# Optimization experiments

Hardware: AMD Instinct MI355X
Metric: run time of the kernel (lower is better)

Reference implementation:

```python
import jax, jax.numpy as jnp
import numpy as np

N_NODES = 50000
IN_NF = 64
HID = 128
OUT_NF = 64
EDGE_HID = HID // 2  # edge_nf_ratio = 2
N_LAYERS = 4
N_EDGES = 800000
NUM_LATENT_NODES = 64
C_EVEN = 1.0
C_ODD = 2.0 / NUM_LATENT_NODES


def setup_inputs() -> dict:
    key = jax.random.key(0)
    ks = jax.random.split(key, 24)
    def lin(k, fan_in, fan_out):
        # torch nn.Linear default init: U(-1/sqrt(fan_in), 1/sqrt(fan_in))
        bound = 1.0 / np.sqrt(fan_in)
        kw, kb = jax.random.split(k)
        w = jax.random.uniform(kw, (fan_in, fan_out), jnp.float32, -bound, bound)
        b = jax.random.uniform(kb, (fan_out,), jnp.float32, -bound, bound)
        return w, b

    h = jax.random.normal(ks[0], (N_NODES, IN_NF), jnp.float32)
    edges_a = jax.random.randint(ks[1], (2, N_EDGES), 0, N_NODES, jnp.int32)
    edges_b = jax.random.randint(ks[2], (2, N_EDGES), 0, N_NODES, jnp.int32)
    update_mask_a = jax.random.randint(ks[3], (N_NODES, 1), 0, 2, jnp.int32).astype(bool)
    update_mask_b = jax.random.randint(ks[4], (N_NODES, 1), 0, 2, jnp.int32).astype(bool)

    emb_in_w, emb_in_b = lin(ks[5], IN_NF, HID)
    emb_out_w, emb_out_b = lin(ks[6], HID, OUT_NF)

    ew1, eb1, ew2, eb2 = [], [], [], []
    nw1, nb1, nw2, nb2 = [], [], [], []
    for i in range(N_LAYERS):
        w, b = lin(ks[7 + i], 2 * HID, EDGE_HID); ew1.append(w); eb1.append(b)
        w, b = lin(ks[11 + i], EDGE_HID, EDGE_HID); ew2.append(w); eb2.append(b)
        w, b = lin(ks[15 + i], HID + EDGE_HID, HID); nw1.append(w); nb1.append(b)
        w, b = lin(ks[19 + i], HID, HID); nw2.append(w); nb2.append(b)

    stack = lambda xs: jnp.stack(xs, 0)
    return {
        "h": h, "edges_a": edges_a, "edges_b": edges_b,
        "update_mask_a": update_mask_a, "update_mask_b": update_mask_b,
        "emb_in_w": emb_in_w, "emb_in_b": emb_in_b,
        "emb_out_w": emb_out_w, "emb_out_b": emb_out_b,
        "edge_w1": stack(ew1), "edge_b1": stack(eb1),
        "edge_w2": stack(ew2), "edge_b2": stack(eb2),
        "node_w1": stack(nw1), "node_b1": stack(nb1),
        "node_w2": stack(nw2), "node_b2": stack(nb2),
    }


def _gcl(h, edges, mask, C, ew1, eb1, ew2, eb2, nw1, nb1, nw2, nb2):
    row, col = edges[0], edges[1]
    # edge model: gather source/target node feats -> 2-layer SiLU MLP
    feat = jnp.concatenate([h[row], h[col]], axis=-1)      # [E, 2*HID]
    m = jax.nn.silu(feat @ ew1 + eb1)                      # [E, EDGE_HID]
    m = jax.nn.silu(m @ ew2 + eb2)                         # [E, EDGE_HID]
    # aggregate messages to receiving nodes (scatter-add), scaled by C
    agg = jax.ops.segment_sum(m, row, num_segments=h.shape[0]) * C
    # node model with residual
    upd = jax.nn.silu(jnp.concatenate([h, agg], axis=-1) @ nw1 + nb1) @ nw2 + nb2
    h_new = h + upd
    # masked asynchronous update: only nodes with mask=True are updated
    return jnp.where(mask, h_new, h)


def reference(h, edges_a, edges_b, update_mask_a, update_mask_b,
              emb_in_w, emb_in_b, emb_out_w, emb_out_b,
              edge_w1, edge_b1, edge_w2, edge_b2,
              node_w1, node_b1, node_w2, node_b2):
    h = h @ emb_in_w + emb_in_b
    for i in range(N_LAYERS):
        if i % 2 == 0:
            edges, mask, C = edges_a, update_mask_a, C_EVEN
        else:
            edges, mask, C = edges_b, update_mask_b, C_ODD
        h = _gcl(h, edges, mask, C,
                 edge_w1[i], edge_b1[i], edge_w2[i], edge_b2[i],
                 node_w1[i], node_b1[i], node_w2[i], node_b2[i])
    h = h @ emb_out_w + emb_out_b
    return h
```

## Files before the change

### kernel.cpp

```cpp
#include <hip/hip_runtime.h>
#include <cstdint>

typedef __bf16 bf16_t;
typedef bf16_t bf16x8 __attribute__((ext_vector_type(8)));
typedef float floatx4 __attribute__((ext_vector_type(4)));
typedef unsigned short ushort4v __attribute__((ext_vector_type(4)));

constexpr int N_NODES = 50000;
constexpr int N_EDGES = 800000;
constexpr int HID = 128;
constexpr int EH = 64;
constexpr int NCH = (N_NODES + 255) / 256;

__device__ __forceinline__ float silu_f(float x) {
    return x * __builtin_amdgcn_rcpf(1.0f + __expf(-x));
}

__global__ __launch_bounds__(256) void pack_all_kernel(
    const float* __restrict__ embin, const float* __restrict__ embout,
    const float* __restrict__ ew1, const float* __restrict__ ew2,
    const float* __restrict__ nw1, const float* __restrict__ nw2,
    bf16_t* __restrict__ pk)
{
    int t = blockIdx.x * 256 + threadIdx.x;
    const float* W; int K, Nc; int base; bf16_t* out;
    if (t < 1024)       { W = embin;  K = 64;  Nc = 128; base = 0;     out = pk; }
    else if (t < 2048)  { W = embout; K = 128; Nc = 64;  base = 1024;  out = pk + 8192; }
    else if (t < 10240) { W = ew1;    K = 256; Nc = 64;  base = 2048;  out = pk + 16384; }
    else if (t < 12288) { W = ew2;    K = 64;  Nc = 64;  base = 10240; out = pk + 81920; }
    else if (t < 24576) { W = nw1;    K = 192; Nc = 128; base = 12288; out = pk + 98304; }
    else                { W = nw2;    K = 128; Nc = 128; base = 24576; out = pk + 196608; }
    t -= base;
    int KS = K >> 5, NT = Nc >> 4;
    int lane = t & 63;
    int chunk = t >> 6;
    int ks = chunk % KS;
    int nt = (chunk / KS) % NT;
    int l  = chunk / (KS * NT);
    int quad = lane >> 4, coln = lane & 15;
    const float* Wl = W + l * K * Nc;
    bf16x8 v;
#pragma unroll
    for (int j = 0; j < 8; j++)
        v[j] = (bf16_t)Wl[(ks * 32 + quad * 8 + j) * Nc + nt * 16 + coln];
    *(bf16x8*)(out + t * 8) = v;
}

__global__ void hist2_kernel(const int* __restrict__ ea, const int* __restrict__ eb,
                             const int* __restrict__ ma, const int* __restrict__ mb,
                             int* __restrict__ ba, int* __restrict__ bb) {
    int half = gridDim.x >> 1;
    int b = blockIdx.x;
    const int* erows; const int* mask; int* bins;
    if (b < half) { erows = ea; mask = ma; bins = ba; }
    else          { erows = eb; mask = mb; bins = bb; b -= half; }
    int i = b * 256 + threadIdx.x;
    if (i >= N_EDGES) return;
    int r = erows[i];
    if (mask[r] != 0) atomicAdd(&bins[r], 1);
}

__global__ __launch_bounds__(256) void scan_phase1(
    const int* __restrict__ bins_a, const int* __restrict__ bins_b,
    int* __restrict__ bs_a, int* __restrict__ bs_b) {
    const int* bins = blockIdx.y ? bins_b : bins_a;
    int* bs = blockIdx.y ? bs_b : bs_a;
    int i = blockIdx.x * 256 + threadIdx.x;
    int v = (i < N_NODES) ? (bins[i] != 0 ? bins[i] : 0) : 0;
#pragma unroll
    for (int off = 32; off; off >>= 1) v += __shfl_down(v, off, 64);
    __shared__ int ws_[4];
    int lane = threadIdx.x & 63, wv = threadIdx.x >> 6;
    if (lane == 0) ws_[wv] = v;
    __syncthreads();
    if (threadIdx.x == 0) bs[blockIdx.x] = ws_[0] + ws_[1] + ws_[2] + ws_[3];
}

__global__ __launch_bounds__(256) void scan_phase2(
    int* __restrict__ bs_a, int* __restrict__ bs_b,
    int* __restrict__ bins_a, int* __restrict__ bins_b) {
    int* bs = blockIdx.x ? bs_b : bs_a;
    int* bins = blockIdx.x ? bins_b : bins_a;
    int t = threadIdx.x, lane = t & 63, wv = t >> 6;
    int v = (t < NCH) ? bs[t] : 0;
    int s = v;
#pragma unroll
    for (int off = 1; off < 64; off <<= 1) {
        int u = __shfl_up(s, off, 64);
        if (lane >= off) s += u;
    }
    __shared__ int wsum[4];
    if (lane == 63) wsum[wv] = s;
    __syncthreads();
    int woff = 0;
    for (int w = 0; w < wv; w++) woff += wsum[w];
    int excl = s - v + woff;
    if (t < NCH) bs[t] = excl;
    if (t == NCH - 1) bins[N_NODES] = excl + v;
}

__global__ __launch_bounds__(256) void mask_scan2(
    int* __restrict__ ms_a, int* __restrict__ ms_b,
    int* __restrict__ cnt_a, int* __restrict__ cnt_b) {
    int* ms = blockIdx.x ? ms_b : ms_a;
    int* cnt = blockIdx.x ? cnt_b : cnt_a;
    int t = threadIdx.x, lane = t & 63, wv = t >> 6;
    int v = (t < NCH) ? ms[t] : 0;
    int s = v;
#pragma unroll
    for (int off = 1; off < 64; off <<= 1) {
        int u = __shfl_up(s, off, 64);
        if (lane >= off) s += u;
    }
    __shared__ int wsum[4];
    if (lane == 63) wsum[wv] = s;
    __syncthreads();
    int woff = 0;
    for (int w = 0; w < wv; w++) woff += wsum[w];
    int excl = s - v + woff;
    if (t < NCH) ms[t] = excl;
    if (t == NCH - 1) cnt[0] = excl + v;
}

__global__ __launch_bounds__(256) void compact_kernel(
    const int* __restrict__ ma, const int* __restrict__ mb,
    const int* __restrict__ ms_a, const int* __restrict__ ms_b,
    int* __restrict__ la, int* __restrict__ lb) {
    const int* mask = blockIdx.y ? mb : ma;
    const int* ms = blockIdx.y ? ms_b : ms_a;
    int* list = blockIdx.y ? lb : la;
    int i = blockIdx.x * 256 + threadIdx.x;
    int t = threadIdx.x, lane = t & 63, wv = t >> 6;
    int m = (i < N_NODES) ? (mask[i] != 0) : 0;
    unsigned long long bal = __ballot(m != 0);
    int pos = (int)__popcll(bal & ((1ull << lane) - 1ull));
    __shared__ int wsum[4];
    if (lane == 63) wsum[wv] = pos + m;
    __syncthreads();
    int woff = 0;
    for (int w = 0; w < wv; w++) woff += wsum[w];
    if (m) list[ms[blockIdx.x] + woff + pos] = i;
}

__global__ __launch_bounds__(256) void scan_phase3(
    int* __restrict__ bins_a, int* __restrict__ bins_b,
    const int* __restrict__ bs_a, const int* __restrict__ bs_b) {
    int* bins = blockIdx.y ? bins_b : bins_a;
    const int* bs = blockIdx.y ? bs_b : bs_a;
    int i = blockIdx.x * 256 + threadIdx.x;
    int t = threadIdx.x, lane = t & 63, wv = t >> 6;
    int v = (i < N_NODES) ? bins[i] : 0;
    int s = v;
#pragma unroll
    for (int off = 1; off < 64; off <<= 1) {
        int u = __shfl_up(s, off, 64);
        if (lane >= off) s += u;
    }
    __shared__ int wsum[4];
    if (lane == 63) wsum[wv] = s;
    __syncthreads();
    int woff = 0;
    for (int w = 0; w < wv; w++) woff += wsum[w];
    if (i < N_NODES) bins[i] = s - v + woff + bs[blockIdx.x];
}

__global__ void fill_src_kernel(const int* __restrict__ bins_a, const int* __restrict__ bins_b,
                                int* __restrict__ ssrc_a, int* __restrict__ ssrc_b) {
    const int* bins = blockIdx.y ? bins_b : bins_a;
    int* ssrc = blockIdx.y ? ssrc_b : ssrc_a;
    int r = blockIdx.x * 256 + threadIdx.x;
    if (r >= N_NODES) return;
    int p0 = bins[r], p1 = bins[r + 1];
    for (int p = p0; p < p1; p++) ssrc[p] = r;
}

__global__ void scatter2_kernel(const int* __restrict__ ea, const int* __restrict__ eb,
                                const int* __restrict__ ma, const int* __restrict__ mb,
                                int* __restrict__ ba, int* __restrict__ bb,
                                int* __restrict__ sdst_a, int* __restrict__ sdst_b) {
    int half = gridDim.x >> 1;
    int b = blockIdx.x;
    const int* e; const int* mask; int* bins; int* sdst;
    if (b < half) { e = ea; mask = ma; bins = ba; sdst = sdst_a; }
    else          { e = eb; mask = mb; bins = bb; sdst = sdst_b; b -= half; }
    int i = b * 256 + threadIdx.x;
    if (i >= N_EDGES) return;
    int r = e[i];
    if (mask[r] == 0) return;
    int c = e[N_EDGES + i];
    int pos = atomicAdd(&bins[r], 1);
    sdst[pos] = c;
}

__global__ __launch_bounds__(256) void emb_in_kernel(
    const float* __restrict__ h0, const bf16_t* __restrict__ wp,
    const float* __restrict__ bias, float* __restrict__ h, bf16_t* __restrict__ h_bf)
{
    int t = threadIdx.x, wave = t >> 6, lane = t & 63;
    int quad = lane >> 4, col = lane & 15;
    int m0 = blockIdx.x * 64 + wave * 16;
    int ndc = min(m0 + col, N_NODES - 1);
    floatx4 acc[8] = {};
#pragma unroll
    for (int ks = 0; ks < 2; ks++) {
        const float* ap = h0 + ndc * 64 + ks * 32 + quad * 8;
        floatx4 f0 = *(const floatx4*)ap;
        floatx4 f1 = *(const floatx4*)(ap + 4);
        bf16x8 a;
#pragma unroll
        for (int j = 0; j < 4; j++) { a[j] = (bf16_t)f0[j]; a[j + 4] = (bf16_t)f1[j]; }
#pragma unroll
        for (int nt = 0; nt < 8; nt++) {
            bf16x8 b = ((const bf16x8*)wp)[(nt * 2 + ks) * 64 + lane];
            acc[nt] = __builtin_amdgcn_mfma_f32_16x16x32_bf16(a, b, acc[nt], 0, 0, 0);
        }
    }
#pragma unroll
    for (int r = 0; r < 4; r++) {
        int nd2 = m0 + quad * 4 + r;
        if (nd2 < N_NODES) {
#pragma unroll
            for (int nt = 0; nt < 8; nt++) {
                int n = nt * 16 + col;
                float x = acc[nt][r] + bias[n];
                h[nd2 * HID + n] = x;
                h_bf[nd2 * HID + n] = (bf16_t)x;
            }
        }
    }
}

__global__ __launch_bounds__(256, 3) void edge_kernel_sorted(
    const bf16_t* __restrict__ h_bf, const int* __restrict__ ssrc,
    const int* __restrict__ sdst, const int* __restrict__ m_ptr,
    const bf16_t* __restrict__ w1p, const float* __restrict__ b1,
    const bf16_t* __restrict__ w2p, const float* __restrict__ b2,
    float* __restrict__ agg, float C)
{
    __shared__ __align__(16) bf16_t w1s[16384];
    __shared__ __align__(16) bf16_t pool[4][64 * 40];

    int t = threadIdx.x;
#pragma unroll
    for (int i = 0; i < 8; i++)
        ((bf16x8*)w1s)[t + 256 * i] = ((const bf16x8*)w1p)[t + 256 * i];
    __syncthreads();

    int wave = t >> 6, lane = t & 63, quad = lane >> 4, col = lane & 15;
    bf16_t* hl = pool[wave];
    bf16_t* mbT = pool[wave];

    float b1v[4], b2v[4];
#pragma unroll
    for (int nt = 0; nt < 4; nt++) { b1v[nt] = b1[nt * 16 + col]; b2v[nt] = b2[nt * 16 + col]; }

    int M = m_ptr[0];
    int ntiles = (M + 31) >> 5;
    int wid = blockIdx.x * 4 + wave, nw = gridDim.x * 4;
    if (wid >= ntiles) return;

    int sr = 0x7fffffff, ds = 0x7fffffff;
    { int p = wid * 32 + lane; if (lane < 32 && p < M) { sr = ssrc[p]; ds = sdst[p]; } }
    bf16x8 a[2][8];
    {
        int ns0 = min(__shfl(sr, col, 64), N_NODES - 1);
        int ns1 = min(__shfl(sr, 16 + col, 64), N_NODES - 1);
        int nd0 = min(__shfl(ds, col, 64), N_NODES - 1);
        int nd1 = min(__shfl(ds, 16 + col, 64), N_NODES - 1);
#pragma unroll
        for (int ks = 0; ks < 8; ks++) {
            int o = (ks & 3) * 32 + quad * 8;
            a[0][ks] = *(const bf16x8*)(h_bf + (ks < 4 ? ns0 : nd0) * HID + o);
            a[1][ks] = *(const bf16x8*)(h_bf + (ks < 4 ? ns1 : nd1) * HID + o);
        }
    }

    for (int tile = wid; tile < ntiles; tile += nw) {
        int tnc = min(tile + nw, ntiles - 1);
        int srn = 0x7fffffff, dsn = 0x7fffffff;
        { int p = tnc * 32 + lane; if (lane < 32 && p < M) { srn = ssrc[p]; dsn = sdst[p]; } }

        floatx4 acc[2][4] = {};
#pragma unroll
        for (int ks = 0; ks < 8; ks++) {
#pragma unroll
            for (int nt = 0; nt < 4; nt++) {
                bf16x8 b = ((const bf16x8*)w1s)[(nt * 8 + ks) * 64 + lane];
                acc[0][nt] = __builtin_amdgcn_mfma_f32_16x16x32_bf16(a[0][ks], b, acc[0][nt], 0, 0, 0);
                acc[1][nt] = __builtin_amdgcn_mfma_f32_16x16x32_bf16(a[1][ks], b, acc[1][nt], 0, 0, 0);
            }
        }

        bf16x8 an[2][8];
        {
            int ns0 = min(__shfl(srn, col, 64), N_NODES - 1);
            int ns1 = min(__shfl(srn, 16 + col, 64), N_NODES - 1);
            int nd0 = min(__shfl(dsn, col, 64), N_NODES - 1);
            int nd1 = min(__shfl(dsn, 16 + col, 64), N_NODES - 1);
#pragma unroll
            for (int ks = 0; ks < 8; ks++) {
                int o = (ks & 3) * 32 + quad * 8;
                an[0][ks] = *(const bf16x8*)(h_bf + (ks < 4 ? ns0 : nd0) * HID + o);
                an[1][ks] = *(const bf16x8*)(h_bf + (ks < 4 ? ns1 : nd1) * HID + o);
            }
        }

#pragma unroll
        for (int m = 0; m < 2; m++)
#pragma unroll
            for (int nt = 0; nt < 4; nt++)
#pragma unroll
                for (int r = 0; r < 4; r++)
                    hl[(m * 16 + quad * 4 + r) * 72 + nt * 16 + col] =
                        (bf16_t)silu_f(acc[m][nt][r] + b1v[nt]);

        floatx4 acc2[2][4] = {};
#pragma unroll
        for (int ks = 0; ks < 2; ks++) {
            bf16x8 a2[2];
#pragma unroll
            for (int m = 0; m < 2; m++)
                a2[m] = *(const bf16x8*)(hl + (m * 16 + col) * 72 + ks * 32 + quad * 8);
#pragma unroll
            for (int nt = 0; nt < 4; nt++) {
                bf16x8 b = ((const bf16x8*)w2p)[(nt * 2 + ks) * 64 + lane];
                acc2[0][nt] = __builtin_amdgcn_mfma_f32_16x16x32_bf16(a2[0], b, acc2[0][nt], 0, 0, 0);
                acc2[1][nt] = __builtin_amdgcn_mfma_f32_16x16x32_bf16(a2[1], b, acc2[1][nt], 0, 0, 0);
            }
        }
#pragma unroll
        for (int m = 0; m < 2; m++)
#pragma unroll
            for (int nt = 0; nt < 4; nt++) {
                ushort4v p;
#pragma unroll
                for (int r = 0; r < 4; r++) {
                    bf16_t bv = (bf16_t)(silu_f(acc2[m][nt][r] + b2v[nt]) * C);
                    p[r] = __builtin_bit_cast(unsigned short, bv);
                }
                *(ushort4v*)(mbT + (nt * 16 + col) * 40 + m * 16 + quad * 4) = p;
            }

        {
            float mv[32];
#pragma unroll
            for (int i = 0; i < 4; i++) {
                bf16x8 v8 = *(const bf16x8*)(mbT + lane * 40 + i * 8);
#pragma unroll
                for (int j = 0; j < 8; j++) mv[i * 8 + j] = (float)v8[j];
            }
            int dp = __shfl(sr, 0, 64);
            float run = mv[0];
#pragma unroll
            for (int r = 1; r < 32; r++) {
                int d = __shfl(sr, r, 64);
                if (d != dp) {
                    if (dp < N_NODES) atomicAdd(agg + dp * EH + lane, run);
                    run = mv[r]; dp = d;
                } else run += mv[r];
            }
            if (dp < N_NODES) atomicAdd(agg + dp * EH + lane, run);
        }

        sr = srn; ds = dsn;
#pragma unroll
        for (int m = 0; m < 2; m++)
#pragma unroll
            for (int ks = 0; ks < 8; ks++) a[m][ks] = an[m][ks];
    }
}

__global__ __launch_bounds__(256) void edge_kernel(
    const bf16_t* __restrict__ h_bf, const int* __restrict__ edges,
    const int* __restrict__ mask,
    const bf16_t* __restrict__ w1p, const float* __restrict__ b1,
    const bf16_t* __restrict__ w2p, const float* __restrict__ b2,
    float* __restrict__ agg, float C)
{
    __shared__ __align__(16) bf16_t w1s[16384];
    __shared__ __align__(16) bf16_t w2s[4096];
    __shared__ __align__(16) bf16_t hl[4][16 * 72];

    int t = threadIdx.x;
#pragma unroll
    for (int i = 0; i < 8; i++)
        ((bf16x8*)w1s)[t + 256 * i] = ((const bf16x8*)w1p)[t + 256 * i];
#pragma unroll
    for (int i = 0; i < 2; i++)
        ((bf16x8*)w2s)[t + 256 * i] = ((const bf16x8*)w2p)[t + 256 * i];
    __syncthreads();

    int wave = t >> 6, lane = t & 63, quad = lane >> 4, col = lane & 15;
    bf16_t* myhl = hl[wave];

    float b1v[4], b2v[4];
#pragma unroll
    for (int nt = 0; nt < 4; nt++) { b1v[nt] = b1[nt * 16 + col]; b2v[nt] = b2[nt * 16 + col]; }

    const int ntile_cnt = N_EDGES / 64;
    for (int tile = blockIdx.x; tile < ntile_cnt; tile += gridDim.x) {
        int ebase = tile * 64 + wave * 16;
        int src = edges[ebase + col];
        int dst = edges[N_EDGES + ebase + col];

        floatx4 acc[4] = {};
#pragma unroll
        for (int ks = 0; ks < 8; ks++) {
            int idx = (ks < 4) ? src : dst;
            bf16x8 a = *(const bf16x8*)(h_bf + idx * HID + (ks & 3) * 32 + quad * 8);
#pragma unroll
            for (int nt = 0; nt < 4; nt++) {
                bf16x8 b = ((const bf16x8*)w1s)[(nt * 8 + ks) * 64 + lane];
                acc[nt] = __builtin_amdgcn_mfma_f32_16x16x32_bf16(a, b, acc[nt], 0, 0, 0);
            }
        }
#pragma unroll
        for (int nt = 0; nt < 4; nt++)
#pragma unroll
            for (int r = 0; r < 4; r++)
                myhl[(quad * 4 + r) * 72 + nt * 16 + col] = (bf16_t)silu_f(acc[nt][r] + b1v[nt]);
        __syncthreads();

        floatx4 acc2[4] = {};
#pragma unroll
        for (int ks = 0; ks < 2; ks++) {
            bf16x8 a = *(const bf16x8*)(myhl + col * 72 + ks * 32 + quad * 8);
#pragma unroll
            for (int nt = 0; nt < 4; nt++) {
                bf16x8 b = ((const bf16x8*)w2s)[(nt * 2 + ks) * 64 + lane];
                acc2[nt] = __builtin_amdgcn_mfma_f32_16x16x32_bf16(a, b, acc2[nt], 0, 0, 0);
            }
        }
#pragma unroll
        for (int r = 0; r < 4; r++) {
            int dest = edges[ebase + quad * 4 + r];
            if (mask[dest] != 0) {
                float* aggp = agg + dest * EH;
#pragma unroll
                for (int nt = 0; nt < 4; nt++) {
                    float x = acc2[nt][r] + b2v[nt];
                    atomicAdd(aggp + nt * 16 + col, silu_f(x) * C);
                }
            }
        }
        __syncthreads();
    }
}

__global__ __launch_bounds__(256) void node_kernel_masked(
    float* __restrict__ h, bf16_t* __restrict__ h_bf,
    float* __restrict__ agg, const int* __restrict__ list,
    const int* __restrict__ cnt_ptr,
    const bf16_t* __restrict__ w1p, const float* __restrict__ b1,
    const bf16_t* __restrict__ w2p, const float* __restrict__ b2)
{
    __shared__ __align__(16) bf16_t hl[4][16 * 136];
    int t = threadIdx.x, wave = t >> 6, lane = t & 63;
    int quad = lane >> 4, col = lane & 15;
    int cnt = cnt_ptr[0];
    int m0 = blockIdx.x * 64 + wave * 16;
    if (m0 >= cnt) return;
    int lv = list[min(m0 + col, cnt - 1)];
    int ndc = lv;

    floatx4 acc[8] = {};
#pragma unroll
    for (int ks = 0; ks < 6; ks++) {
        bf16x8 a;
        if (ks < 4) {
            a = *(const bf16x8*)(h_bf + ndc * HID + ks * 32 + quad * 8);
        } else {
            const float* ap = agg + ndc * EH + (ks - 4) * 32 + quad * 8;
            floatx4 f0 = *(const floatx4*)ap;
            floatx4 f1 = *(const floatx4*)(ap + 4);
#pragma unroll
            for (int j = 0; j < 4; j++) { a[j] = (bf16_t)f0[j]; a[j + 4] = (bf16_t)f1[j]; }
        }
#pragma unroll
        for (int nt = 0; nt < 8; nt++) {
            bf16x8 b = ((const bf16x8*)w1p)[(nt * 6 + ks) * 64 + lane];
            acc[nt] = __builtin_amdgcn_mfma_f32_16x16x32_bf16(a, b, acc[nt], 0, 0, 0);
        }
    }
    if ((m0 + col) < cnt) {
        floatx4 z = {0.0f, 0.0f, 0.0f, 0.0f};
        float* zp = agg + ndc * EH + quad * 8;
        *(floatx4*)zp = z; *(floatx4*)(zp + 4) = z;
        *(floatx4*)(zp + 32) = z; *(floatx4*)(zp + 36) = z;
    }
    bf16_t* myhl = hl[wave];
#pragma unroll
    for (int nt = 0; nt < 8; nt++)
#pragma unroll
        for (int r = 0; r < 4; r++) {
            float x = acc[nt][r] + b1[nt * 16 + col];
            myhl[(quad * 4 + r) * 136 + nt * 16 + col] = (bf16_t)silu_f(x);
        }

    floatx4 acc2[8] = {};
#pragma unroll
    for (int ks = 0; ks < 4; ks++) {
        bf16x8 a = *(const bf16x8*)(myhl + col * 136 + ks * 32 + quad * 8);
#pragma unroll
        for (int nt = 0; nt < 8; nt++) {
            bf16x8 b = ((const bf16x8*)w2p)[(nt * 4 + ks) * 64 + lane];
            acc2[nt] = __builtin_amdgcn_mfma_f32_16x16x32_bf16(a, b, acc2[nt], 0, 0, 0);
        }
    }
#pragma unroll
    for (int r = 0; r < 4; r++) {
        if ((m0 + quad * 4 + r) < cnt) {
            int nd2 = __shfl(lv, quad * 4 + r, 64);
#pragma unroll
            for (int nt = 0; nt < 8; nt++) {
                int n = nt * 16 + col;
                float hv = h[nd2 * HID + n] + acc2[nt][r] + b2[n];
                h[nd2 * HID + n] = hv;
                h_bf[nd2 * HID + n] = (bf16_t)hv;
            }
        }
    }
}

__global__ __launch_bounds__(256) void node_kernel(
    float* __restrict__ h, bf16_t* __restrict__ h_bf,
    float* __restrict__ agg, const int* __restrict__ mask,
    const bf16_t* __restrict__ w1p, const float* __restrict__ b1,
    const bf16_t* __restrict__ w2p, const float* __restrict__ b2,
    const bf16_t* __restrict__ wop, const float* __restrict__ bo,
    float* __restrict__ out)
{
    __shared__ __align__(16) bf16_t hl[4][16 * 136];
    int t = threadIdx.x, wave = t >> 6, lane = t & 63;
    int quad = lane >> 4, col = lane & 15;
    int m0 = blockIdx.x * 64 + wave * 16;
    int ndc = min(m0 + col, N_NODES - 1);

    floatx4 acc[8] = {};
#pragma unroll
    for (int ks = 0; ks < 6; ks++) {
        bf16x8 a;
        if (ks < 4) {
            a = *(const bf16x8*)(h_bf + ndc * HID + ks * 32 + quad * 8);
        } else {
            const float* ap = agg + ndc * EH + (ks - 4) * 32 + quad * 8;
            floatx4 f0 = *(const floatx4*)ap;
            floatx4 f1 = *(const floatx4*)(ap + 4);
#pragma unroll
            for (int j = 0; j < 4; j++) { a[j] = (bf16_t)f0[j]; a[j + 4] = (bf16_t)f1[j]; }
        }
#pragma unroll
        for (int nt = 0; nt < 8; nt++) {
            bf16x8 b = ((const bf16x8*)w1p)[(nt * 6 + ks) * 64 + lane];
            acc[nt] = __builtin_amdgcn_mfma_f32_16x16x32_bf16(a, b, acc[nt], 0, 0, 0);
        }
    }
    bf16_t* myhl = hl[wave];
#pragma unroll
    for (int nt = 0; nt < 8; nt++)
#pragma unroll
        for (int r = 0; r < 4; r++) {
            float x = acc[nt][r] + b1[nt * 16 + col];
            myhl[(quad * 4 + r) * 136 + nt * 16 + col] = (bf16_t)silu_f(x);
        }

    floatx4 acc2[8] = {};
#pragma unroll
    for (int ks = 0; ks < 4; ks++) {
        bf16x8 a = *(const bf16x8*)(myhl + col * 136 + ks * 32 + quad * 8);
#pragma unroll
        for (int nt = 0; nt < 8; nt++) {
            bf16x8 b = ((const bf16x8*)w2p)[(nt * 4 + ks) * 64 + lane];
            acc2[nt] = __builtin_amdgcn_mfma_f32_16x16x32_bf16(a, b, acc2[nt], 0, 0, 0);
        }
    }
#pragma unroll
    for (int r = 0; r < 4; r++) {
        int nd2 = m0 + quad * 4 + r;
        bool valid = nd2 < N_NODES;
        bool upd = valid && mask[min(nd2, N_NODES - 1)] != 0;
        if (upd) {
#pragma unroll
            for (int nt = 0; nt < 8; nt++) {
                int n = nt * 16 + col;
                float hv = h[nd2 * HID + n] + acc2[nt][r] + b2[n];
                h[nd2 * HID + n] = hv;
                bf16_t hb = (bf16_t)hv;
                h_bf[nd2 * HID + n] = hb;
                myhl[(quad * 4 + r) * 136 + n] = hb;
            }
        } else {
#pragma unroll
            for (int nt = 0; nt < 8; nt++) {
                int n = nt * 16 + col;
                myhl[(quad * 4 + r) * 136 + n] =
                    valid ? h_bf[nd2 * HID + n] : (bf16_t)0.0f;
            }
        }
    }
    floatx4 ao[4] = {};
#pragma unroll
    for (int ks = 0; ks < 4; ks++) {
        bf16x8 a = *(const bf16x8*)(myhl + col * 136 + ks * 32 + quad * 8);
#pragma unroll
        for (int nt = 0; nt < 4; nt++) {
            bf16x8 b = ((const bf16x8*)wop)[(nt * 4 + ks) * 64 + lane];
            ao[nt] = __builtin_amdgcn_mfma_f32_16x16x32_bf16(a, b, ao[nt], 0, 0, 0);
        }
    }
#pragma unroll
    for (int r = 0; r < 4; r++) {
        int nd2 = m0 + quad * 4 + r;
        if (nd2 < N_NODES) {
#pragma unroll
            for (int nt = 0; nt < 4; nt++) {
                int n = nt * 16 + col;
                out[nd2 * 64 + n] = ao[nt][r] + bo[n];
            }
        }
    }
}

extern "C" void kernel_launch(void* const* d_in, const int* in_sizes, int n_in,
                              void* d_out, int out_size, void* d_ws, size_t ws_size,
                              hipStream_t stream) {
    const float* h0        = (const float*)d_in[0];
    const int*   edges_a   = (const int*)d_in[1];
    const int*   edges_b   = (const int*)d_in[2];
    const int*   mask_a    = (const int*)d_in[3];
    const int*   mask_b    = (const int*)d_in[4];
    const float* emb_in_w  = (const float*)d_in[5];
    const float* emb_in_b  = (const float*)d_in[6];
    const float* emb_out_w = (const float*)d_in[7];
    const float* emb_out_b = (const float*)d_in[8];
    const float* ew1 = (const float*)d_in[9];
    const float* eb1 = (const float*)d_in[10];
    const float* ew2 = (const float*)d_in[11];
    const float* eb2 = (const float*)d_in[12];
    const float* nw1 = (const float*)d_in[13];
    const float* nb1 = (const float*)d_in[14];
    const float* nw2 = (const float*)d_in[15];
    const float* nb2 = (const float*)d_in[16];

    const size_t SZ_H = 25600000, SZ_HBF = 12800000, SZ_AGG = 12800000, SZ_PK = 524288;
    const size_t SZ_S = 3200000, SZ_BINS = 200704, SZ_BS = 1024, SZ_LIST = 200704;

    char* ws = (char*)d_ws;
    size_t off = 0;
    float*  h    = (float*)(ws + off);  off += SZ_H;
    bf16_t* h_bf = (bf16_t*)(ws + off); off += SZ_HBF;
    float*  agg  = (float*)(ws + off);  off += SZ_AGG;
    bf16_t* pk   = (bf16_t*)(ws + off); off += SZ_PK;
    int* ssrc_a = (int*)(ws + off); off += SZ_S;
    int* sdst_a = (int*)(ws + off); off += SZ_S;
    int* ssrc_b = (int*)(ws + off); off += SZ_S;
    int* sdst_b = (int*)(ws + off); off += SZ_S;
    int* bins_a = (int*)(ws + off); off += SZ_BINS;
    int* bins_b = (int*)(ws + off); off += SZ_BINS;
    int* bs_a   = (int*)(ws + off); off += SZ_BS;
    int* bs_b   = (int*)(ws + off); off += SZ_BS;
    int* ms_a   = (int*)(ws + off); off += SZ_BS;
    int* ms_b   = (int*)(ws + off); off += SZ_BS;
    int* cnt_a  = (int*)(ws + off); off += 256;
    int* cnt_b  = (int*)(ws + off); off += 256;
    int* list_a = (int*)(ws + off); off += SZ_LIST;
    int* list_b = (int*)(ws + off); off += SZ_LIST;
    bool sorted_path = (ws_size >= off);

    bf16_t* pk_embin  = pk;
    bf16_t* pk_embout = pk + 8192;
    bf16_t* pk_ew1    = pk + 16384;
    bf16_t* pk_ew2    = pk + 81920;
    bf16_t* pk_nw1    = pk + 98304;
    bf16_t* pk_nw2    = pk + 196608;

    pack_all_kernel<<<128, 256, 0, stream>>>(emb_in_w, emb_out_w, ew1, ew2, nw1, nw2, pk);

    const int edge_grid = (N_EDGES + 255) / 256;
    const int node_blocks = (N_NODES + 63) / 64;
    if (sorted_path) {
        hipMemsetAsync(bins_a, 0, 2 * SZ_BINS + 2 * SZ_BS, stream);
        hist2_kernel<<<2 * edge_grid, 256, 0, stream>>>(edges_a, edges_b, mask_a, mask_b,
                                                        bins_a, bins_b);
        scan_phase1<<<dim3(NCH, 2), 256, 0, stream>>>(bins_a, bins_b, bs_a, bs_b);
        scan_phase2<<<2, 256, 0, stream>>>(bs_a, bs_b, bins_a, bins_b);
        scan_phase3<<<dim3(NCH, 2), 256, 0, stream>>>(bins_a, bins_b, bs_a, bs_b);
        fill_src_kernel<<<dim3(NCH, 2), 256, 0, stream>>>(bins_a, bins_b, ssrc_a, ssrc_b);
        scatter2_kernel<<<2 * edge_grid, 256, 0, stream>>>(edges_a, edges_b, mask_a, mask_b,
                                                           bins_a, bins_b, sdst_a, sdst_b);
        scan_phase1<<<dim3(NCH, 2), 256, 0, stream>>>(mask_a, mask_b, ms_a, ms_b);
        mask_scan2<<<2, 256, 0, stream>>>(ms_a, ms_b, cnt_a, cnt_b);
        compact_kernel<<<dim3(NCH, 2), 256, 0, stream>>>(mask_a, mask_b, ms_a, ms_b,
                                                         list_a, list_b);
    }

    hipMemsetAsync(agg, 0, (size_t)N_NODES * EH * 4, stream);
    emb_in_kernel<<<node_blocks, 256, 0, stream>>>(h0, pk_embin, emb_in_b, h, h_bf);

    for (int l = 0; l < 4; l++) {
        const int* mask = (l & 1) ? mask_b : mask_a;
        float C = (l & 1) ? 0.03125f : 1.0f;
        if (sorted_path) {
            const int* ssrc = (l & 1) ? ssrc_b : ssrc_a;
            const int* sdst = (l & 1) ? sdst_b : sdst_a;
            const int* mp   = ((l & 1) ? bins_b : bins_a) + N_NODES;
            edge_kernel_sorted<<<768, 256, 0, stream>>>(h_bf, ssrc, sdst, mp,
                                                        pk_ew1 + l * 16384, eb1 + l * 64,
                                                        pk_ew2 + l * 4096,  eb2 + l * 64,
                                                        agg, C);
        } else {
            const int* edges = (l & 1) ? edges_b : edges_a;
            edge_kernel<<<768, 256, 0, stream>>>(h_bf, edges, mask,
                                                 pk_ew1 + l * 16384, eb1 + l * 64,
                                                 pk_ew2 + l * 4096,  eb2 + l * 64,
                                                 agg, C);
        }
        if (l < 3 && sorted_path) {
            const int* list = (l & 1) ? list_b : list_a;
            const int* cnt  = (l & 1) ? cnt_b : cnt_a;
            node_kernel_masked<<<node_blocks, 256, 0, stream>>>(
                h, h_bf, agg, list, cnt,
                pk_nw1 + l * 24576, nb1 + l * 128,
                pk_nw2 + l * 16384, nb2 + l * 128);
        } else if (l < 3) {
            node_kernel<<<node_blocks, 256, 0, stream>>>(h, h_bf, agg, mask,
                                                         pk_nw1 + l * 24576, nb1 + l * 128,
                                                         pk_nw2 + l * 16384, nb2 + l * 128,
                                                         pk_embout, emb_out_b, (float*)d_out);
            hipMemsetAsync(agg, 0, (size_t)N_NODES * EH * 4, stream);
        } else {
            node_kernel<<<node_blocks, 256, 0, stream>>>(h, h_bf, agg, mask,
                                                         pk_nw1 + 3 * 24576, nb1 + 3 * 128,
                                                         pk_nw2 + 3 * 16384, nb2 + 3 * 128,
                                                         pk_embout, emb_out_b, (float*)d_out);
        }
    }
}
```

Before: 444.2 us.

## Precompute per-node first edge-layer projections and gather them per edge

Result: no change. 439.8 us (-1.0%).

```diff
diff --git a/kernel.cpp b/kernel.cpp
--- a/kernel.cpp
+++ b/kernel.cpp
@@ -23,6 +23,20 @@
     bf16_t* __restrict__ pk)
 {
     int t = blockIdx.x * 256 + threadIdx.x;
+    if (t >= 32768) {
+        t -= 32768;
+        int lane = t & 63, chunk = t >> 6;
+        int ks = chunk & 3, nt = (chunk >> 2) & 7, l = chunk >> 5;
+        int quad = lane >> 4, coln = lane & 15;
+        const float* Wl = ew1 + l * 256 * 64;
+        int kb = (nt >= 4 ? 128 : 0) + ks * 32 + quad * 8;
+        int nc = (nt & 3) * 16 + coln;
+        bf16x8 v;
+#pragma unroll
+        for (int j = 0; j < 8; j++) v[j] = (bf16_t)Wl[(kb + j) * 64 + nc];
+        *(bf16x8*)(pk + 262144 + t * 8) = v;
+        return;
+    }
     const float* W; int K, Nc; int base; bf16_t* out;
     if (t < 1024)       { W = embin;  K = 64;  Nc = 128; base = 0;     out = pk; }
     else if (t < 2048)  { W = embout; K = 128; Nc = 64;  base = 1024;  out = pk + 8192; }
@@ -227,6 +241,136 @@
                 h_bf[nd2 * HID + n] = (bf16_t)x;
             }
         }
+    }
+}
+
+__global__ __launch_bounds__(256) void pre_edge_kernel(
+    const bf16_t* __restrict__ h_bf, const bf16_t* __restrict__ w1cat,
+    const float* __restrict__ b1, float* __restrict__ P)
+{
+    int t = threadIdx.x, wave = t >> 6, lane = t & 63;
+    int quad = lane >> 4, col = lane & 15;
+    int m0 = blockIdx.x * 64 + wave * 16;
+    int ndc = min(m0 + col, N_NODES - 1);
+    floatx4 acc[8] = {};
+#pragma unroll
+    for (int ks = 0; ks < 4; ks++) {
+        bf16x8 a = *(const bf16x8*)(h_bf + ndc * HID + ks * 32 + quad * 8);
+#pragma unroll
+        for (int nt = 0; nt < 8; nt++) {
+            bf16x8 b = ((const bf16x8*)w1cat)[(nt * 4 + ks) * 64 + lane];
+            acc[nt] = __builtin_amdgcn_mfma_f32_16x16x32_bf16(a, b, acc[nt], 0, 0, 0);
+        }
+    }
+#pragma unroll
+    for (int r = 0; r < 4; r++) {
+        int nd2 = m0 + quad * 4 + r;
+        if (nd2 < N_NODES) {
+#pragma unroll
+            for (int nt = 0; nt < 8; nt++) {
+                int n = nt * 16 + col;
+                float x = acc[nt][r] + (nt >= 4 ? b1[n - 64] : 0.0f);
+                P[nd2 * 128 + n] = x;
+            }
+        }
+    }
+}
+
+__global__ __launch_bounds__(256, 4) void edge_kernel_pre(
+    const float* __restrict__ P, const int* __restrict__ ssrc,
+    const int* __restrict__ sdst, const int* __restrict__ m_ptr,
+    const bf16_t* __restrict__ w2p, const float* __restrict__ b2,
+    float* __restrict__ agg, float C)
+{
+    __shared__ __align__(16) bf16_t pool[4][64 * 40];
+
+    int t = threadIdx.x;
+    int wave = t >> 6, lane = t & 63, quad = lane >> 4, col = lane & 15;
+    bf16_t* mbT = pool[wave];
+
+    float b2v[4];
+#pragma unroll
+    for (int nt = 0; nt < 4; nt++) b2v[nt] = b2[nt * 16 + col];
+
+    int M = m_ptr[0];
+    int ntiles = (M + 31) >> 5;
+    int wid = blockIdx.x * 4 + wave, nw = gridDim.x * 4;
+    if (wid >= ntiles) return;
+
+    int sr = 0x7fffffff, ds = 0x7fffffff;
+    { int p = wid * 32 + lane; if (lane < 32 && p < M) { sr = ssrc[p]; ds = sdst[p]; } }
+
+    for (int tile = wid; tile < ntiles; tile += nw) {
+        int tnc = min(tile + nw, ntiles - 1);
+        int srn = 0x7fffffff, dsn = 0x7fffffff;
+        { int p = tnc * 32 + lane; if (lane < 32 && p < M) { srn = ssrc[p]; dsn = sdst[p]; } }
+
+        floatx4 acc2[2][4] = {};
+#pragma unroll
+        for (int m = 0; m < 2; m++) {
+            int rN = min(__shfl(sr, m * 16 + col, 64), N_NODES - 1);
+            int cN = min(__shfl(ds, m * 16 + col, 64), N_NODES - 1);
+            const float* pr = P + rN * 128 + quad * 8;
+            const float* pc = P + cN * 128 + 64 + quad * 8;
+            floatx4 fr[4], fc[4];
+#pragma unroll
+            for (int ks = 0; ks < 2; ks++) {
+                fr[ks * 2]     = *(const floatx4*)(pr + ks * 32);
+                fr[ks * 2 + 1] = *(const floatx4*)(pr + ks * 32 + 4);
+                fc[ks * 2]     = *(const floatx4*)(pc + ks * 32);
+                fc[ks * 2 + 1] = *(const floatx4*)(pc + ks * 32 + 4);
+            }
+#pragma unroll
+            for (int ks = 0; ks < 2; ks++) {
+                bf16x8 a2;
+#pragma unroll
+                for (int j = 0; j < 4; j++) {
+                    a2[j]     = (bf16_t)silu_f(fr[ks * 2][j]     + fc[ks * 2][j]);
+                    a2[j + 4] = (bf16_t)silu_f(fr[ks * 2 + 1][j] + fc[ks * 2 + 1][j]);
+                }
+#pragma unroll
+                for (int nt = 0; nt < 4; nt++) {
+                    bf16x8 b = ((const bf16x8*)w2p)[(nt * 2 + ks) * 64 + lane];
+                    acc2[m][nt] = __builtin_amdgcn_mfma_f32_16x16x32_bf16(a2, b, acc2[m][nt], 0, 0, 0);
+                }
+            }
+        }
+
+#pragma unroll
+        for (int m = 0; m < 2; m++)
+#pragma unroll
+            for (int nt = 0; nt < 4; nt++) {
+                ushort4v pv;
+#pragma unroll
+                for (int r = 0; r < 4; r++) {
+                    bf16_t bv = (bf16_t)(silu_f(acc2[m][nt][r] + b2v[nt]) * C);
+                    pv[r] = __builtin_bit_cast(unsigned short, bv);
+                }
+                *(ushort4v*)(mbT + (nt * 16 + col) * 40 + m * 16 + quad * 4) = pv;
+            }
+
+        {
+            float mv[32];
+#pragma unroll
+            for (int i = 0; i < 4; i++) {
+                bf16x8 v8 = *(const bf16x8*)(mbT + lane * 40 + i * 8);
+#pragma unroll
+                for (int j = 0; j < 8; j++) mv[i * 8 + j] = (float)v8[j];
+            }
+            int dp = __shfl(sr, 0, 64);
+            float run = mv[0];
+#pragma unroll
+            for (int r = 1; r < 32; r++) {
+                int d = __shfl(sr, r, 64);
+                if (d != dp) {
+                    if (dp < N_NODES) atomicAdd(agg + dp * EH + lane, run);
+                    run = mv[r]; dp = d;
+                } else run += mv[r];
+            }
+            if (dp < N_NODES) atomicAdd(agg + dp * EH + lane, run);
+        }
+
+        sr = srn; ds = dsn;
     }
 }
 
@@ -642,8 +786,10 @@
     const float* nw2 = (const float*)d_in[15];
     const float* nb2 = (const float*)d_in[16];
 
-    const size_t SZ_H = 25600000, SZ_HBF = 12800000, SZ_AGG = 12800000, SZ_PK = 524288;
+    const size_t SZ_H = 25600000, SZ_HBF = 12800000, SZ_AGG = 12800000;
+    const size_t SZ_PK = 655360;
     const size_t SZ_S = 3200000, SZ_BINS = 200704, SZ_BS = 1024, SZ_LIST = 200704;
+    const size_t SZ_P = 25600000;
 
     char* ws = (char*)d_ws;
     size_t off = 0;
@@ -666,6 +812,8 @@
     int* list_a = (int*)(ws + off); off += SZ_LIST;
     int* list_b = (int*)(ws + off); off += SZ_LIST;
     bool sorted_path = (ws_size >= off);
+    float* P = (float*)(ws + off); off += SZ_P;
+    bool pre_path = (ws_size >= off);
 
     bf16_t* pk_embin  = pk;
     bf16_t* pk_embout = pk + 8192;
@@ -673,8 +821,9 @@
     bf16_t* pk_ew2    = pk + 81920;
     bf16_t* pk_nw1    = pk + 98304;
     bf16_t* pk_nw2    = pk + 196608;
-
-    pack_all_kernel<<<128, 256, 0, stream>>>(emb_in_w, emb_out_w, ew1, ew2, nw1, nw2, pk);
+    bf16_t* pk_ew1cat = pk + 262144;
+
+    pack_all_kernel<<<160, 256, 0, stream>>>(emb_in_w, emb_out_w, ew1, ew2, nw1, nw2, pk);
 
     const int edge_grid = (N_EDGES + 255) / 256;
     const int node_blocks = (N_NODES + 63) / 64;
@@ -700,7 +849,16 @@
     for (int l = 0; l < 4; l++) {
         const int* mask = (l & 1) ? mask_b : mask_a;
         float C = (l & 1) ? 0.03125f : 1.0f;
-        if (sorted_path) {
+        if (pre_path) {
+            const int* ssrc = (l & 1) ? ssrc_b : ssrc_a;
+            const int* sdst = (l & 1) ? sdst_b : sdst_a;
+            const int* mp   = ((l & 1) ? bins_b : bins_a) + N_NODES;
+            pre_edge_kernel<<<node_blocks, 256, 0, stream>>>(
+                h_bf, pk_ew1cat + l * 16384, eb1 + l * 64, P);
+            edge_kernel_pre<<<1024, 256, 0, stream>>>(P, ssrc, sdst, mp,
+                                                      pk_ew2 + l * 4096, eb2 + l * 64,
+                                                      agg, C);
+        } else if (sorted_path) {
             const int* ssrc = (l & 1) ? ssrc_b : ssrc_a;
             const int* sdst = (l & 1) ? sdst_b : sdst_a;
             const int* mp   = ((l & 1) ? bins_b : bins_a) + N_NODES;
```
